# Optimization experiments

Hardware: AMD Instinct MI355X
Metric: run time of the kernel (lower is better)

The kernel has to match this reference:

```python
import jax, jax.numpy as jnp
import numpy as np

B, N, D, H = 2, 2048, 1024, 16
HD = D // H
SCALE = 1.0 / float(np.sqrt(HD))


def _cx(r, i):
    return (r + 1j * i).astype(jnp.complex64)


def setup_inputs() -> dict:
    key = jax.random.key(0)
    ks = jax.random.split(key, 20)
    inp = {
        "Z_r": jax.random.normal(ks[0], (B, N, D), jnp.float32),
        "Z_i": jax.random.normal(ks[1], (B, N, D), jnp.float32),
    }
    i = 2
    w_scale = 0.02
    for nm in ("q", "k", "v", "o"):
        inp[f"w{nm}_r"] = jax.random.normal(ks[i], (D, D), jnp.float32) * w_scale
        inp[f"w{nm}_i"] = jax.random.normal(ks[i + 1], (D, D), jnp.float32) * w_scale
        inp[f"b{nm}_r"] = jax.random.normal(ks[i + 2], (D,), jnp.float32) * w_scale
        inp[f"b{nm}_i"] = jax.random.normal(ks[i + 3], (D,), jnp.float32) * w_scale
        i += 4
    inp["mask"] = jax.random.randint(ks[18], (B, N), 0, 2, jnp.int32)
    return inp


def reference(Z_r, Z_i, wq_r, wq_i, bq_r, bq_i, wk_r, wk_i, bk_r, bk_i,
              wv_r, wv_i, bv_r, bv_i, wo_r, wo_i, bo_r, bo_i, mask):
    Z = _cx(Z_r, Z_i)  # (B,N,D) complex64

    def lin(x, wr, wi, br, bi):  # complex nn.Linear: x @ W^T + b
        return x @ _cx(wr, wi).T + _cx(br, bi)

    def heads(x):  # (B,N,D) -> (B,H,N,HD)
        return x.reshape(B, N, H, HD).transpose(0, 2, 1, 3)

    q = heads(lin(Z, wq_r, wq_i, bq_r, bq_i))
    k = heads(lin(Z, wk_r, wk_i, bk_r, bk_i))
    v = heads(lin(Z, wv_r, wv_i, bv_r, bv_i))

    # Re(q @ k^T) with plain transpose (no conjugate), as in the torch code:
    # Re = qr.kr^T - qi.ki^T  (computed directly on real parts, no wasted imag GEMM)
    scores = (jnp.einsum('bhnd,bhmd->bhnm', q.real, k.real)
              - jnp.einsum('bhnd,bhmd->bhnm', q.imag, k.imag)) * SCALE
    scores = jnp.where(mask[:, None, None, :] == 0, jnp.float32(-1e9), scores)
    w = jax.nn.softmax(scores, axis=-1)  # (B,H,N,N) real

    # complex output: real weights times complex V -> apply to real/imag separately
    out_r = jnp.einsum('bhnm,bhmd->bhnd', w, v.real)
    out_i = jnp.einsum('bhnm,bhmd->bhnd', w, v.imag)
    out = _cx(out_r, out_i).transpose(0, 2, 1, 3).reshape(B, N, D)

    y = Z + lin(out, wo_r, wo_i, bo_r, bo_i)
    # return real/imag stacked as float32: (2,B,N,D)
    return jnp.stack([y.real, y.imag])
```

## Files before the change

kernel.cpp:

```cpp
#include <hip/hip_runtime.h>
#include <math.h>

#define BB 2
#define NN 2048
#define DD 1024
#define KA 2048
#define HH 16
#define HD 64
#define MM (BB*NN)
#define SCALE 0.125f
#define NT (KA/32)

typedef __attribute__((ext_vector_type(8))) short bf16x8;
typedef __attribute__((ext_vector_type(4))) short bf16x4;
typedef __attribute__((ext_vector_type(4))) float f32x4;

#define MFMA(a,b,c) __builtin_amdgcn_mfma_f32_16x16x32_bf16(a,b,c,0,0,0)

__device__ __forceinline__ unsigned short f2bf(float x) {
    union { float f; unsigned u; } v; v.f = x;
    unsigned r = v.u + 0x7FFFu + ((v.u >> 16) & 1u);
    return (unsigned short)(r >> 16);
}

__device__ __forceinline__ void async16(void* l, const void* g) {
    __builtin_amdgcn_global_load_lds(
        (const __attribute__((address_space(1))) unsigned int*)g,
        (__attribute__((address_space(3))) unsigned int*)l, 16, 0, 0);
}

__device__ __forceinline__ bf16x8 ld8s(const short* p) {
    bf16x4 lo = *(const bf16x4*)p;
    bf16x4 hi = *(const bf16x4*)(p + 4);
    bf16x8 r;
    r[0]=lo[0]; r[1]=lo[1]; r[2]=lo[2]; r[3]=lo[3];
    r[4]=hi[0]; r[5]=hi[1]; r[6]=hi[2]; r[7]=hi[3];
    return r;
}
__device__ __forceinline__ void st8s(short* p, bf16x8 v) {
    bf16x4 lo, hi;
    lo[0]=v[0]; lo[1]=v[1]; lo[2]=v[2]; lo[3]=v[3];
    hi[0]=v[4]; hi[1]=v[5]; hi[2]=v[6]; hi[3]=v[7];
    *(bf16x4*)p = lo;
    *(bf16x4*)(p + 4) = hi;
}

__global__ __launch_bounds__(256) void mask_scan(const int* __restrict__ mask,
                                                 int* __restrict__ idxArr,
                                                 int* __restrict__ cntArr)
{
    const int b = blockIdx.x, t = threadIdx.x;
    __shared__ int part[256];
    int m[8]; int c = 0;
#pragma unroll
    for (int j = 0; j < 8; j++) { m[j] = mask[b*NN + t*8 + j]; c += (m[j] != 0); }
    part[t] = c; __syncthreads();
    for (int off = 1; off < 256; off <<= 1) {
        int v = (t >= off) ? part[t - off] : 0;
        __syncthreads();
        part[t] += v;
        __syncthreads();
    }
    int base = part[t] - c;
    int total = part[255];
#pragma unroll
    for (int j = 0; j < 8; j++) if (m[j]) idxArr[b*NN + base++] = t*8 + j;
    for (int p = total + t; p < NN; p += 256) idxArr[b*NN + p] = 0;
    if (t == 0) cntArr[b] = total;
}

__global__ __launch_bounds__(256) void cvt_aug(
    const float* __restrict__ Zr, const float* __restrict__ Zi,
    const float* __restrict__ wqr, const float* __restrict__ wqi,
    const float* __restrict__ wkr, const float* __restrict__ wki,
    const float* __restrict__ wvr, const float* __restrict__ wvi,
    const float* __restrict__ wor, const float* __restrict__ woi,
    unsigned short* __restrict__ Zaug,
    unsigned short* __restrict__ Wqa, unsigned short* __restrict__ Wka,
    unsigned short* __restrict__ Wva, unsigned short* __restrict__ Woa)
{
    const int bid = blockIdx.x, t = threadIdx.x;
    const int col = t * 8;
    const float* src;
    float sgn = 1.0f;
    unsigned short* dst;

    if (bid < 4096) {
        const int m = bid;
        src = (col < 1024) ? (Zr + (size_t)m*1024 + col) : (Zi + (size_t)m*1024 + col - 1024);
        dst = Zaug + (size_t)m * KA + col;
    } else {
        const int w = (bid - 4096) >> 11;
        const int r = (bid - 4096) & 2047;
        const int o = r & 1023;
        const float *wr_, *wi_;
        unsigned short* wa;
        switch (w) {
            case 0: wr_ = wqr; wi_ = wqi; wa = Wqa; break;
            case 1: wr_ = wkr; wi_ = wki; wa = Wka; break;
            case 2: wr_ = wvr; wi_ = wvi; wa = Wva; break;
            default: wr_ = wor; wi_ = woi; wa = Woa; break;
        }
        const bool imagrow = (r >= 1024);
        if (!imagrow) {
            if (col < 1024) { src = wr_ + (size_t)o*1024 + col; sgn = 1.0f; }
            else            { src = wi_ + (size_t)o*1024 + col - 1024; sgn = -1.0f; }
        } else {
            const float s = (w == 1) ? -1.0f : 1.0f;
            if (col < 1024) { src = wi_ + (size_t)o*1024 + col; sgn = s; }
            else            { src = wr_ + (size_t)o*1024 + col - 1024; sgn = s; }
        }
        dst = wa + (size_t)r * KA + col;
    }

    float4 a = *(const float4*)src;
    float4 b4 = *(const float4*)(src + 4);
    bf16x8 o8;
    o8[0]=(short)f2bf(sgn*a.x); o8[1]=(short)f2bf(sgn*a.y);
    o8[2]=(short)f2bf(sgn*a.z); o8[3]=(short)f2bf(sgn*a.w);
    o8[4]=(short)f2bf(sgn*b4.x); o8[5]=(short)f2bf(sgn*b4.y);
    o8[6]=(short)f2bf(sgn*b4.z); o8[7]=(short)f2bf(sgn*b4.w);
    *(bf16x8*)dst = o8;
}

__global__ __launch_bounds__(256) void proj_all(
    const unsigned short* __restrict__ Zaug,
    const unsigned short* __restrict__ Wqa, const unsigned short* __restrict__ Wka,
    const unsigned short* __restrict__ Wva,
    const float* __restrict__ bqr, const float* __restrict__ bqi,
    const float* __restrict__ bkr, const float* __restrict__ bki,
    const float* __restrict__ bvr, const float* __restrict__ bvi,
    const int* __restrict__ idxArr, const int* __restrict__ cntArr,
    unsigned short* __restrict__ Qr, unsigned short* __restrict__ Qi,
    unsigned short* __restrict__ Krc, unsigned short* __restrict__ nKic,
    unsigned short* __restrict__ Vtr, unsigned short* __restrict__ Vti)
{
    const int gx = blockIdx.x;
    int slice, b = 0, m0c;
    const unsigned short* wsel;
    const float *br, *bi;
    if (gx < 32) {
        slice = 0; m0c = gx * 128;
        wsel = Wqa; br = bqr; bi = bqi;
    } else if (gx < 64) {
        slice = 1; int t = gx - 32; b = t >> 4; m0c = (t & 15) * 128;
        wsel = Wka; br = bkr; bi = bki;
    } else {
        slice = 2; int t = gx - 64; b = t >> 4; m0c = (t & 15) * 128;
        wsel = Wva; br = bvr; bi = bvi;
    }
    if (slice != 0) {
        const int cnt = cntArr[b];
        if (m0c >= ((cnt + 63) & ~63)) return;
    }

    __shared__ __align__(16) short S[3][2][128][32];
    __shared__ int idx_s[128];

    const int tid = threadIdx.x;
    const int lane = tid & 63, wave = tid >> 6;
    const int lr = lane & 15, lg = lane >> 4;
    const int wrow = (wave >> 1) * 64, wcol = (wave & 1) * 64;
    const int o0 = blockIdx.y * 128;

    if (tid < 128)
        idx_s[tid] = (slice == 0) ? (m0c + tid) : (b*NN + idxArr[b*NN + m0c + tid]);
    __syncthreads();

    const int rsub = lane >> 2;
    const int csrc = (((lane & 3) ^ ((lane >> 3) & 3)) * 8);

    const unsigned short* gp[4];
    int lpo[4];
#pragma unroll
    for (int i = 0; i < 4; i++) {
        const int s = i * 4 + wave;
        if (s < 8) {
            const int row = s * 16 + rsub;
            gp[i] = Zaug + (size_t)idx_s[row] * KA + csrc;
            lpo[i] = s * 1024 + lane * 16;
        } else {
            const int row = (s - 8) * 16 + rsub;
            gp[i] = wsel + (size_t)(o0 + row) * KA + csrc;
            lpo[i] = 8192 + (s - 8) * 1024 + lane * 16;
        }
    }

    f32x4 acc[4][4];
#pragma unroll
    for (int m = 0; m < 4; m++)
#pragma unroll
        for (int n = 0; n < 4; n++) acc[m][n] = (f32x4){0.f,0.f,0.f,0.f};

#pragma unroll
    for (int i = 0; i < 4; i++) { async16((char*)S + lpo[i], gp[i]); gp[i] += 32; }
#pragma unroll
    for (int i = 0; i < 4; i++) { async16((char*)S + 16384 + lpo[i], gp[i]); gp[i] += 32; }

    const int kb = ((lg ^ ((lr >> 1) & 3)) * 8);

    int cur = 0, stg = 2;
    for (int t = 0; t < NT - 1; t++) {
        asm volatile("s_waitcnt vmcnt(4)" ::: "memory");
        __builtin_amdgcn_s_barrier();
        __builtin_amdgcn_sched_barrier(0);

        if (t + 2 < NT) {
            char* nb = (char*)S + stg * 16384;
#pragma unroll
            for (int i = 0; i < 4; i++) { async16(nb + lpo[i], gp[i]); gp[i] += 32; }
        }

        const short (*Sa)[32] = (const short (*)[32])((const char*)S + cur * 16384);
        const short (*Sb)[32] = Sa + 128;
        bf16x8 af[4], bw[4];
#pragma unroll
        for (int m = 0; m < 4; m++) af[m] = *(const bf16x8*)&Sa[wrow + m*16 + lr][kb];
#pragma unroll
        for (int n = 0; n < 4; n++) bw[n] = *(const bf16x8*)&Sb[wcol + n*16 + lr][kb];
#pragma unroll
        for (int m = 0; m < 4; m++)
#pragma unroll
            for (int n = 0; n < 4; n++) acc[m][n] = MFMA(af[m], bw[n], acc[m][n]);

        cur = (cur == 2) ? 0 : cur + 1;
        stg = (stg == 2) ? 0 : stg + 1;
    }
    asm volatile("s_waitcnt vmcnt(0)" ::: "memory");
    __builtin_amdgcn_s_barrier();
    __builtin_amdgcn_sched_barrier(0);
    {
        const short (*Sa)[32] = (const short (*)[32])((const char*)S + cur * 16384);
        const short (*Sb)[32] = Sa + 128;
        bf16x8 af[4], bw[4];
#pragma unroll
        for (int m = 0; m < 4; m++) af[m] = *(const bf16x8*)&Sa[wrow + m*16 + lr][kb];
#pragma unroll
        for (int n = 0; n < 4; n++) bw[n] = *(const bf16x8*)&Sb[wcol + n*16 + lr][kb];
#pragma unroll
        for (int m = 0; m < 4; m++)
#pragma unroll
            for (int n = 0; n < 4; n++) acc[m][n] = MFMA(af[m], bw[n], acc[m][n]);
    }

#pragma unroll
    for (int mi = 0; mi < 4; mi++)
#pragma unroll
        for (int nj = 0; nj < 4; nj++) {
            const int o = o0 + wcol + nj*16 + lr;
            const int half = o >> 10;
            const int oc = o & 1023;
            const int h = oc >> 6, hd = oc & 63;
            const float bias = half ? ((slice == 1) ? -bi[oc] : bi[oc]) : br[oc];
            if (slice == 2) {
                bf16x4 p4;
#pragma unroll
                for (int reg = 0; reg < 4; reg++)
                    p4[reg] = (short)f2bf(acc[mi][nj][reg] + bias);
                const int jc = m0c + wrow + mi*16 + lg*4;
                size_t base = ((size_t)((b*HH + h)*HD + hd)) * NN + jc;
                if (half) *(bf16x4*)&Vti[base] = p4;
                else      *(bf16x4*)&Vtr[base] = p4;
            } else if (slice == 1) {
                unsigned short* dst = half ? nKic : Krc;
#pragma unroll
                for (int reg = 0; reg < 4; reg++) {
                    const int jc = m0c + wrow + mi*16 + lg*4 + reg;
                    dst[((size_t)((b*HH + h)*NN + jc)) * HD + hd] =
                        f2bf(acc[mi][nj][reg] + bias);
                }
            } else {
                unsigned short* dst = half ? Qi : Qr;
#pragma unroll
                for (int reg = 0; reg < 4; reg++) {
                    const int m = m0c + wrow + mi*16 + lg*4 + reg;
                    const int b2 = m >> 11, n = m & (NN - 1);
                    dst[((size_t)((b2*HH + h)*NN + n)) * HD + hd] =
                        f2bf((acc[mi][nj][reg] + bias) * SCALE);
                }
            }
        }
}

#define LDP 72
__global__ __launch_bounds__(256) void attn_mfma(
    const unsigned short* __restrict__ Qr, const unsigned short* __restrict__ Qi,
    const unsigned short* __restrict__ Krc, const unsigned short* __restrict__ nKic,
    const unsigned short* __restrict__ Vtc, const unsigned short* __restrict__ Vtic,
    const int* __restrict__ cntArr,
    unsigned short* __restrict__ Aaug)
{
    __shared__ short Kr_s[64][LDP], Ki_s[64][LDP], Vr_s[64][LDP], Vi_s[64][LDP];
    __shared__ short P_s[4][32][LDP];

    const int tid = threadIdx.x;
    const int lane = tid & 63, wave = tid >> 6;
    const int lr = lane & 15, lg = lane >> 4;
    const int h = blockIdx.y, b = blockIdx.z;
    const int n0 = blockIdx.x * 128 + wave * 32;
    const size_t qb = ((size_t)(b*HH + h)) * NN * HD;
    const int cnt = cntArr[b];
    const int ct = (cnt + 63) & ~63;

    bf16x8 qr[2][2], qi[2][2];
#pragma unroll
    for (int mf = 0; mf < 2; mf++)
#pragma unroll
        for (int kf = 0; kf < 2; kf++) {
            qr[mf][kf] = *(const bf16x8*)&Qr[qb + (size_t)(n0 + mf*16 + lr) * HD + kf*32 + lg*8];
            qi[mf][kf] = *(const bf16x8*)&Qi[qb + (size_t)(n0 + mf*16 + lr) * HD + kf*32 + lg*8];
        }

    f32x4 o_r[2][4], o_i[2][4];
#pragma unroll
    for (int mf = 0; mf < 2; mf++)
#pragma unroll
        for (int nf = 0; nf < 4; nf++) {
            o_r[mf][nf] = (f32x4){0.f,0.f,0.f,0.f};
            o_i[mf][nf] = (f32x4){0.f,0.f,0.f,0.f};
        }
    float m_run[2][4], l_run[2][4];
#pragma unroll
    for (int mf = 0; mf < 2; mf++)
#pragma unroll
        for (int r = 0; r < 4; r++) { m_run[mf][r] = -3.0e38f; l_run[mf][r] = 0.0f; }

    for (int t0 = 0; t0 < ct; t0 += 64) {
        __syncthreads();
        for (int c = tid; c < 512; c += 256) {
            int row = c >> 3, ch = (c & 7) * 8;
            st8s(&Kr_s[row][ch], *(const bf16x8*)&Krc [qb + (size_t)(t0 + row) * HD + ch]);
            st8s(&Ki_s[row][ch], *(const bf16x8*)&nKic[qb + (size_t)(t0 + row) * HD + ch]);
            st8s(&Vr_s[row][ch], *(const bf16x8*)&Vtc [qb + (size_t)row * NN + t0 + ch]);
            st8s(&Vi_s[row][ch], *(const bf16x8*)&Vtic[qb + (size_t)row * NN + t0 + ch]);
        }
        __syncthreads();

        f32x4 sacc[2][4];
#pragma unroll
        for (int nf = 0; nf < 4; nf++) {
            bf16x8 k0f = ld8s(&Kr_s[nf*16 + lr][lg*8]);
            bf16x8 k1f = ld8s(&Kr_s[nf*16 + lr][32 + lg*8]);
            bf16x8 i0f = ld8s(&Ki_s[nf*16 + lr][lg*8]);
            bf16x8 i1f = ld8s(&Ki_s[nf*16 + lr][32 + lg*8]);
#pragma unroll
            for (int mf = 0; mf < 2; mf++) {
                f32x4 a = (f32x4){0.f,0.f,0.f,0.f};
                a = MFMA(qr[mf][0], k0f, a);
                a = MFMA(qr[mf][1], k1f, a);
                a = MFMA(qi[mf][0], i0f, a);
                a = MFMA(qi[mf][1], i1f, a);
                sacc[mf][nf] = a;
            }
        }

        if (t0 + 64 > cnt) {
#pragma unroll
            for (int nf = 0; nf < 4; nf++) {
                if (t0 + nf*16 + lr >= cnt) {
#pragma unroll
                    for (int mf = 0; mf < 2; mf++)
#pragma unroll
                        for (int r = 0; r < 4; r++) sacc[mf][nf][r] = -1e9f;
                }
            }
        }

#pragma unroll
        for (int mf = 0; mf < 2; mf++) {
            float fac[4];
#pragma unroll
            for (int r = 0; r < 4; r++) {
                float v = fmaxf(fmaxf(sacc[mf][0][r], sacc[mf][1][r]),
                                fmaxf(sacc[mf][2][r], sacc[mf][3][r]));
                v = fmaxf(v, __shfl_xor(v, 1, 64));
                v = fmaxf(v, __shfl_xor(v, 2, 64));
                v = fmaxf(v, __shfl_xor(v, 4, 64));
                v = fmaxf(v, __shfl_xor(v, 8, 64));
                float mn = fmaxf(m_run[mf][r], v);
                fac[r] = __expf(m_run[mf][r] - mn);
                m_run[mf][r] = mn;
            }
            float psum[4] = {0.f, 0.f, 0.f, 0.f};
#pragma unroll
            for (int nf = 0; nf < 4; nf++)
#pragma unroll
                for (int r = 0; r < 4; r++) {
                    float p = __expf(sacc[mf][nf][r] - m_run[mf][r]);
                    psum[r] += p;
                    P_s[wave][mf*16 + lg*4 + r][nf*16 + lr] = (short)f2bf(p);
                }
#pragma unroll
            for (int r = 0; r < 4; r++) {
                float ps = psum[r];
                ps += __shfl_xor(ps, 1, 64);
                ps += __shfl_xor(ps, 2, 64);
                ps += __shfl_xor(ps, 4, 64);
                ps += __shfl_xor(ps, 8, 64);
                l_run[mf][r] = l_run[mf][r] * fac[r] + ps;
            }
#pragma unroll
            for (int nf = 0; nf < 4; nf++)
#pragma unroll
                for (int r = 0; r < 4; r++) {
                    o_r[mf][nf][r] *= fac[r];
                    o_i[mf][nf][r] *= fac[r];
                }
        }
        __syncthreads();

        bf16x8 pa[2][2];
#pragma unroll
        for (int mf = 0; mf < 2; mf++) {
            pa[mf][0] = ld8s(&P_s[wave][mf*16 + lr][lg*8]);
            pa[mf][1] = ld8s(&P_s[wave][mf*16 + lr][32 + lg*8]);
        }
#pragma unroll
        for (int nf = 0; nf < 4; nf++) {
            bf16x8 v0 = ld8s(&Vr_s[nf*16 + lr][lg*8]);
            bf16x8 v1 = ld8s(&Vr_s[nf*16 + lr][32 + lg*8]);
            bf16x8 w0 = ld8s(&Vi_s[nf*16 + lr][lg*8]);
            bf16x8 w1 = ld8s(&Vi_s[nf*16 + lr][32 + lg*8]);
#pragma unroll
            for (int mf = 0; mf < 2; mf++) {
                o_r[mf][nf] = MFMA(pa[mf][0], v0, o_r[mf][nf]);
                o_r[mf][nf] = MFMA(pa[mf][1], v1, o_r[mf][nf]);
                o_i[mf][nf] = MFMA(pa[mf][0], w0, o_i[mf][nf]);
                o_i[mf][nf] = MFMA(pa[mf][1], w1, o_i[mf][nf]);
            }
        }
    }

#pragma unroll
    for (int mf = 0; mf < 2; mf++) {
        float invl[4];
#pragma unroll
        for (int r = 0; r < 4; r++) invl[r] = 1.0f / l_run[mf][r];
#pragma unroll
        for (int nf = 0; nf < 4; nf++)
#pragma unroll
            for (int r = 0; r < 4; r++) {
                int row = n0 + mf*16 + lg*4 + r;
                int col = h*HD + nf*16 + lr;
                size_t o = ((size_t)(b*NN + row)) * KA + col;
                Aaug[o]        = f2bf(o_r[mf][nf][r] * invl[r]);
                Aaug[o + 1024] = f2bf(o_i[mf][nf][r] * invl[r]);
            }
    }
}

__global__ __launch_bounds__(256) void final_mfma(
    const unsigned short* __restrict__ Aaug, const unsigned short* __restrict__ Woa,
    const float* __restrict__ bor, const float* __restrict__ boi,
    const float* __restrict__ Zr, const float* __restrict__ Zi,
    float* __restrict__ out)
{
    __shared__ __align__(16) short S[3][2][128][32];

    const int tid = threadIdx.x;
    const int lane = tid & 63, wave = tid >> 6;
    const int lr = lane & 15, lg = lane >> 4;
    const int wrow = (wave >> 1) * 64, wcol = (wave & 1) * 64;
    const int m0 = blockIdx.x * 128, o0 = blockIdx.y * 128;

    const int rsub = lane >> 2;
    const int csrc = (((lane & 3) ^ ((lane >> 3) & 3)) * 8);

    const unsigned short* gp[4];
    int lpo[4];
#pragma unroll
    for (int i = 0; i < 4; i++) {
        const int s = i * 4 + wave;
        if (s < 8) {
            const int row = s * 16 + rsub;
            gp[i] = Aaug + (size_t)(m0 + row) * KA + csrc;
            lpo[i] = s * 1024 + lane * 16;
        } else {
            const int row = (s - 8) * 16 + rsub;
            gp[i] = Woa + (size_t)(o0 + row) * KA + csrc;
            lpo[i] = 8192 + (s - 8) * 1024 + lane * 16;
        }
    }

    f32x4 acc[4][4];
#pragma unroll
    for (int m = 0; m < 4; m++)
#pragma unroll
        for (int n = 0; n < 4; n++) acc[m][n] = (f32x4){0.f,0.f,0.f,0.f};

#pragma unroll
    for (int i = 0; i < 4; i++) { async16((char*)S + lpo[i], gp[i]); gp[i] += 32; }
#pragma unroll
    for (int i = 0; i < 4; i++) { async16((char*)S + 16384 + lpo[i], gp[i]); gp[i] += 32; }

    const int kb = ((lg ^ ((lr >> 1) & 3)) * 8);

    int cur = 0, stg = 2;
    for (int t = 0; t < NT - 1; t++) {
        asm volatile("s_waitcnt vmcnt(4)" ::: "memory");
        __builtin_amdgcn_s_barrier();
        __builtin_amdgcn_sched_barrier(0);

        if (t + 2 < NT) {
            char* nb = (char*)S + stg * 16384;
#pragma unroll
            for (int i = 0; i < 4; i++) { async16(nb + lpo[i], gp[i]); gp[i] += 32; }
        }

        const short (*Sa)[32] = (const short (*)[32])((const char*)S + cur * 16384);
        const short (*Sb)[32] = Sa + 128;
        bf16x8 af[4], bw[4];
#pragma unroll
        for (int m = 0; m < 4; m++) af[m] = *(const bf16x8*)&Sa[wrow + m*16 + lr][kb];
#pragma unroll
        for (int n = 0; n < 4; n++) bw[n] = *(const bf16x8*)&Sb[wcol + n*16 + lr][kb];
#pragma unroll
        for (int m = 0; m < 4; m++)
#pragma unroll
            for (int n = 0; n < 4; n++) acc[m][n] = MFMA(af[m], bw[n], acc[m][n]);

        cur = (cur == 2) ? 0 : cur + 1;
        stg = (stg == 2) ? 0 : stg + 1;
    }
    asm volatile("s_waitcnt vmcnt(0)" ::: "memory");
    __builtin_amdgcn_s_barrier();
    __builtin_amdgcn_sched_barrier(0);
    {
        const short (*Sa)[32] = (const short (*)[32])((const char*)S + cur * 16384);
        const short (*Sb)[32] = Sa + 128;
        bf16x8 af[4], bw[4];
#pragma unroll
        for (int m = 0; m < 4; m++) af[m] = *(const bf16x8*)&Sa[wrow + m*16 + lr][kb];
#pragma unroll
        for (int n = 0; n < 4; n++) bw[n] = *(const bf16x8*)&Sb[wcol + n*16 + lr][kb];
#pragma unroll
        for (int m = 0; m < 4; m++)
#pragma unroll
            for (int n = 0; n < 4; n++) acc[m][n] = MFMA(af[m], bw[n], acc[m][n]);
    }

#pragma unroll
    for (int mi = 0; mi < 4; mi++)
#pragma unroll
        for (int nj = 0; nj < 4; nj++) {
            const int o = o0 + wcol + nj*16 + lr;
            const int half = o >> 10;
            const int oc = o & 1023;
            const float bias = half ? boi[oc] : bor[oc];
            const float* resid = half ? Zi : Zr;
            float* dst = out + (half ? (size_t)MM * DD : 0);
#pragma unroll
            for (int reg = 0; reg < 4; reg++) {
                const int m = m0 + wrow + mi*16 + lg*4 + reg;
                size_t zi = (size_t)m * DD + oc;
                dst[zi] = acc[mi][nj][reg] + bias + resid[zi];
            }
        }
}

extern "C" void kernel_launch(void* const* d_in, const int* in_sizes, int n_in,
                              void* d_out, int out_size, void* d_ws, size_t ws_size,
                              hipStream_t stream)
{
    const float* Zr  = (const float*)d_in[0];
    const float* Zi  = (const float*)d_in[1];
    const float* wqr = (const float*)d_in[2];
    const float* wqi = (const float*)d_in[3];
    const float* bqr = (const float*)d_in[4];
    const float* bqi = (const float*)d_in[5];
    const float* wkr = (const float*)d_in[6];
    const float* wki = (const float*)d_in[7];
    const float* bkr = (const float*)d_in[8];
    const float* bki = (const float*)d_in[9];
    const float* wvr = (const float*)d_in[10];
    const float* wvi = (const float*)d_in[11];
    const float* bvr = (const float*)d_in[12];
    const float* bvi = (const float*)d_in[13];
    const float* wor = (const float*)d_in[14];
    const float* woi = (const float*)d_in[15];
    const float* bor = (const float*)d_in[16];
    const float* boi = (const float*)d_in[17];
    const int*  mask = (const int*)d_in[18];

    unsigned short* w16 = (unsigned short*)d_ws;
    const size_t ZA = (size_t)MM * KA;
    const size_t WA = (size_t)KA * KA;
    const size_t HN = (size_t)MM * DD;
    unsigned short* Zaug = w16;
    unsigned short* Wqa  = Zaug + ZA;
    unsigned short* Wka  = Wqa + WA;
    unsigned short* Wva  = Wka + WA;
    unsigned short* Woa  = Wva + WA;
    unsigned short* Qr16 = Woa + WA;
    unsigned short* Qi16 = Qr16 + HN;
    unsigned short* Krc16 = Qi16 + HN;
    unsigned short* nKic16 = Krc16 + HN;
    unsigned short* Vtr16 = nKic16 + HN;
    unsigned short* Vti16 = Vtr16 + HN;
    unsigned short* Aaug = Vti16 + HN;
    int* idxArr = (int*)(Aaug + ZA);
    int* cntArr = idxArr + BB * NN;

    mask_scan<<<BB, 256, 0, stream>>>(mask, idxArr, cntArr);

    cvt_aug<<<12288, 256, 0, stream>>>(
        Zr, Zi, wqr, wqi, wkr, wki, wvr, wvi, wor, woi,
        Zaug, Wqa, Wka, Wva, Woa);

    proj_all<<<dim3(96, 16), 256, 0, stream>>>(
        Zaug, Wqa, Wka, Wva,
        bqr, bqi, bkr, bki, bvr, bvi, idxArr, cntArr,
        Qr16, Qi16, Krc16, nKic16, Vtr16, Vti16);

    attn_mfma<<<dim3(NN/128, HH, BB), 256, 0, stream>>>(
        Qr16, Qi16, Krc16, nKic16, Vtr16, Vti16, cntArr, Aaug);

    final_mfma<<<dim3(32, 16), 256, 0, stream>>>(
        Aaug, Woa, bor, boi, Zr, Zi, (float*)d_out);
}
```

Before: 266.3 us.

## Enlarge projection GEMM tile to 256x128 with 64-wide K and single-buffered loads

The QKV projection kernel now computes 256-row by 128-column tiles with a K step of 64, and each wave accumulates 8x4 MFMA fragments instead of 4x4. This raises data reuse per byte loaded and halves the grid. The three-stage async pipeline is replaced by one buffer guarded by two __syncthreads per iteration, so global load latency is no longer overlapped with MFMA work. The larger accumulator set raises register pressure, and the fewer, bigger blocks may leave CUs underfilled.

```diff
diff --git a/kernel.cpp b/kernel.cpp
--- a/kernel.cpp
+++ b/kernel.cpp
@@ -139,14 +139,14 @@
     int slice, b = 0, m0c;
     const unsigned short* wsel;
     const float *br, *bi;
-    if (gx < 32) {
-        slice = 0; m0c = gx * 128;
+    if (gx < 16) {
+        slice = 0; m0c = gx * 256;
         wsel = Wqa; br = bqr; bi = bqi;
-    } else if (gx < 64) {
-        slice = 1; int t = gx - 32; b = t >> 4; m0c = (t & 15) * 128;
+    } else if (gx < 32) {
+        slice = 1; int t = gx - 16; b = t >> 3; m0c = (t & 7) * 256;
         wsel = Wka; br = bkr; bi = bki;
     } else {
-        slice = 2; int t = gx - 64; b = t >> 4; m0c = (t & 15) * 128;
+        slice = 2; int t = gx - 32; b = t >> 3; m0c = (t & 7) * 256;
         wsel = Wva; br = bvr; bi = bvi;
     }
     if (slice != 0) {
@@ -154,97 +154,72 @@
         if (m0c >= ((cnt + 63) & ~63)) return;
     }
 
-    __shared__ __align__(16) short S[3][2][128][32];
-    __shared__ int idx_s[128];
+    __shared__ __align__(16) short S[24576];
+    __shared__ int idx_s[256];
 
     const int tid = threadIdx.x;
     const int lane = tid & 63, wave = tid >> 6;
     const int lr = lane & 15, lg = lane >> 4;
-    const int wrow = (wave >> 1) * 64, wcol = (wave & 1) * 64;
+    const int wrow = (wave >> 1) * 128, wcol = (wave & 1) * 64;
     const int o0 = blockIdx.y * 128;
 
-    if (tid < 128)
-        idx_s[tid] = (slice == 0) ? (m0c + tid) : (b*NN + idxArr[b*NN + m0c + tid]);
+    idx_s[tid] = (slice == 0) ? (m0c + tid) : (b*NN + idxArr[b*NN + m0c + tid]);
     __syncthreads();
 
-    const int rsub = lane >> 2;
-    const int csrc = (((lane & 3) ^ ((lane >> 3) & 3)) * 8);
-
-    const unsigned short* gp[4];
-    int lpo[4];
-#pragma unroll
-    for (int i = 0; i < 4; i++) {
+    const int rsub8 = lane >> 3;
+    const int colo8 = (((lane & 7) ^ rsub8) * 8);
+
+    const unsigned short* gp[12];
+    int lpo[12];
+#pragma unroll
+    for (int i = 0; i < 12; i++) {
         const int s = i * 4 + wave;
-        if (s < 8) {
-            const int row = s * 16 + rsub;
-            gp[i] = Zaug + (size_t)idx_s[row] * KA + csrc;
+        if (s < 32) {
+            const int row = s * 8 + rsub8;
+            gp[i] = Zaug + (size_t)idx_s[row] * KA + colo8;
             lpo[i] = s * 1024 + lane * 16;
         } else {
-            const int row = (s - 8) * 16 + rsub;
-            gp[i] = wsel + (size_t)(o0 + row) * KA + csrc;
-            lpo[i] = 8192 + (s - 8) * 1024 + lane * 16;
-        }
-    }
-
-    f32x4 acc[4][4];
-#pragma unroll
-    for (int m = 0; m < 4; m++)
+            const int row = (s - 32) * 8 + rsub8;
+            gp[i] = wsel + (size_t)(o0 + row) * KA + colo8;
+            lpo[i] = 32768 + (s - 32) * 1024 + lane * 16;
+        }
+    }
+
+    f32x4 acc[8][4];
+#pragma unroll
+    for (int m = 0; m < 8; m++)
 #pragma unroll
         for (int n = 0; n < 4; n++) acc[m][n] = (f32x4){0.f,0.f,0.f,0.f};
 
-#pragma unroll
-    for (int i = 0; i < 4; i++) { async16((char*)S + lpo[i], gp[i]); gp[i] += 32; }
-#pragma unroll
-    for (int i = 0; i < 4; i++) { async16((char*)S + 16384 + lpo[i], gp[i]); gp[i] += 32; }
-
-    const int kb = ((lg ^ ((lr >> 1) & 3)) * 8);
-
-    int cur = 0, stg = 2;
-    for (int t = 0; t < NT - 1; t++) {
-        asm volatile("s_waitcnt vmcnt(4)" ::: "memory");
-        __builtin_amdgcn_s_barrier();
-        __builtin_amdgcn_sched_barrier(0);
-
-        if (t + 2 < NT) {
-            char* nb = (char*)S + stg * 16384;
-#pragma unroll
-            for (int i = 0; i < 4; i++) { async16(nb + lpo[i], gp[i]); gp[i] += 32; }
-        }
-
-        const short (*Sa)[32] = (const short (*)[32])((const char*)S + cur * 16384);
-        const short (*Sb)[32] = Sa + 128;
-        bf16x8 af[4], bw[4];
-#pragma unroll
-        for (int m = 0; m < 4; m++) af[m] = *(const bf16x8*)&Sa[wrow + m*16 + lr][kb];
-#pragma unroll
-        for (int n = 0; n < 4; n++) bw[n] = *(const bf16x8*)&Sb[wcol + n*16 + lr][kb];
-#pragma unroll
-        for (int m = 0; m < 4; m++)
-#pragma unroll
-            for (int n = 0; n < 4; n++) acc[m][n] = MFMA(af[m], bw[n], acc[m][n]);
-
-        cur = (cur == 2) ? 0 : cur + 1;
-        stg = (stg == 2) ? 0 : stg + 1;
-    }
-    asm volatile("s_waitcnt vmcnt(0)" ::: "memory");
-    __builtin_amdgcn_s_barrier();
-    __builtin_amdgcn_sched_barrier(0);
-    {
-        const short (*Sa)[32] = (const short (*)[32])((const char*)S + cur * 16384);
-        const short (*Sb)[32] = Sa + 128;
-        bf16x8 af[4], bw[4];
-#pragma unroll
-        for (int m = 0; m < 4; m++) af[m] = *(const bf16x8*)&Sa[wrow + m*16 + lr][kb];
-#pragma unroll
-        for (int n = 0; n < 4; n++) bw[n] = *(const bf16x8*)&Sb[wcol + n*16 + lr][kb];
-#pragma unroll
-        for (int m = 0; m < 4; m++)
-#pragma unroll
-            for (int n = 0; n < 4; n++) acc[m][n] = MFMA(af[m], bw[n], acc[m][n]);
-    }
-
-#pragma unroll
-    for (int mi = 0; mi < 4; mi++)
+    const short (*Sa)[64] = (const short (*)[64])S;
+    const short (*Sb)[64] = (const short (*)[64])(S + 16384);
+
+    for (int k0 = 0; k0 < KA; k0 += 64) {
+        __syncthreads();
+#pragma unroll
+        for (int i = 0; i < 12; i++) {
+            async16((char*)S + lpo[i], gp[i]);
+            gp[i] += 64;
+        }
+        __syncthreads();
+
+#pragma unroll
+        for (int half = 0; half < 2; half++) {
+            const int kb = ((half * 4 + lg) ^ (lr & 7)) * 8;
+            bf16x8 af[8], bw[4];
+#pragma unroll
+            for (int m = 0; m < 8; m++) af[m] = *(const bf16x8*)&Sa[wrow + m*16 + lr][kb];
+#pragma unroll
+            for (int n = 0; n < 4; n++) bw[n] = *(const bf16x8*)&Sb[wcol + n*16 + lr][kb];
+#pragma unroll
+            for (int m = 0; m < 8; m++)
+#pragma unroll
+                for (int n = 0; n < 4; n++) acc[m][n] = MFMA(af[m], bw[n], acc[m][n]);
+        }
+    }
+
+#pragma unroll
+    for (int mi = 0; mi < 8; mi++)
 #pragma unroll
         for (int nj = 0; nj < 4; nj++) {
             const int o = o0 + wcol + nj*16 + lr;
@@ -607,7 +582,7 @@
         Zr, Zi, wqr, wqi, wkr, wki, wvr, wvi, wor, woi,
         Zaug, Wqa, Wka, Wva, Woa);
 
-    proj_all<<<dim3(96, 16), 256, 0, stream>>>(
+    proj_all<<<dim3(48, 16), 256, 0, stream>>>(
         Zaug, Wqa, Wka, Wva,
         bqr, bqi, bkr, bki, bvr, bvi, idxArr, cntArr,
         Qr16, Qi16, Krc16, nKic16, Vtr16, Vti16);
```

Measured after the change: 341.1 us. 1.28x slower.
